# Optimization experiments

Hardware: AMD Instinct MI355X
Metric: run time of the kernel (lower is better)

The kernel has to match this reference:

```python
import jax, jax.numpy as jnp
import numpy as np

B, N, D = 4, 4096, 1024
HEADS, DIM_HEAD = 16, 64
INNER = HEADS * DIM_HEAD
LN_EPS = 1e-5


def next_fast_len(n):
    # smallest 5-smooth integer >= n (matches scipy.fftpack.next_fast_len)
    while True:
        m = n
        for p in (2, 3, 5):
            while m % p == 0:
                m //= p
        if m == 1:
            return n
        n += 1


def setup_inputs() -> dict:
    key = jax.random.key(0)
    k = jax.random.split(key, 6)
    x = jax.random.normal(k[0], (B, N, D), dtype=jnp.float32)
    gamma = jnp.ones((D,), dtype=jnp.float32)
    beta = jnp.zeros((D,), dtype=jnp.float32)
    alpha = jax.random.normal(k[1], (HEADS,), dtype=jnp.float32)
    w_in = jax.random.normal(k[2], (INNER, D), dtype=jnp.float32) * 0.02
    w_out = jax.random.normal(k[3], (D, INNER), dtype=jnp.float32) * 0.02
    return {"x": x, "gamma": gamma, "beta": beta, "alpha": alpha, "w_in": w_in, "w_out": w_out}


def reference(x, gamma, beta, alpha, w_in, w_out):
    b, n, d = x.shape
    h, dh = HEADS, DIM_HEAD
    # LayerNorm (biased variance, eps=1e-5)
    mu = jnp.mean(x, axis=-1, keepdims=True)
    var = jnp.var(x, axis=-1, keepdims=True)
    xn = (x - mu) * jax.lax.rsqrt(var + LN_EPS) * gamma + beta
    # project_in (no bias), split heads: b n (h d) -> b h n d
    xi = jnp.einsum('bnd,ed->bne', xn, w_in)
    xi = xi.reshape(b, n, h, dh).transpose(0, 2, 1, 3)  # [b,h,n,dh]
    # exponential decay weights per head: alpha * (1-alpha)**flip(arange(n)) -> [h, n]
    a = jax.nn.sigmoid(alpha)[:, None]
    weights = a * (1.0 - a) ** jnp.arange(n - 1, -1, -1, dtype=x.dtype)[None, :]
    # FFT-based causal correlation (conv1d_fft)
    fast_len = next_fast_len(n + n - 1)
    f_x = jnp.fft.rfft(xi, n=fast_len, axis=-2)           # [b,h,L',dh] complex
    f_w = jnp.fft.rfft(weights, n=fast_len, axis=-1)      # [h,L'] complex
    out = jnp.fft.irfft(f_x * jnp.conj(f_w)[None, :, :, None], fast_len, axis=-2)
    out = jnp.roll(out, -1, axis=-2)
    out = out[:, :, fast_len - n:, :]                      # last n positions -> [b,h,n,dh]
    # merge heads and project out
    out = out.transpose(0, 2, 1, 3).reshape(b, n, h * dh)
    return jnp.einsum('bne,de->bnd', out, w_out)
```

## Files before the change

### kernel.cpp

```cpp
#include <hip/hip_runtime.h>
#include <hip/hip_bf16.h>

#define B_ 4
#define N_ 4096
#define D_ 1024
#define H_ 16
#define INNER_ 1024
#define M_ (B_ * N_)
#define CH_ 128
#define CL_ 32

using bf16x8  = __attribute__((ext_vector_type(8))) __bf16;
using f32x4   = __attribute__((ext_vector_type(4))) float;
using f32x16  = __attribute__((ext_vector_type(16))) float;

__device__ __forceinline__ float bf2f(unsigned short v) {
  return __uint_as_float(((unsigned)v) << 16);
}
__device__ __forceinline__ unsigned short f2bf(float f) {
  __hip_bfloat16 h = __float2bfloat16(f);
  return *reinterpret_cast<unsigned short*>(&h);
}
__device__ __forceinline__ float sigm(float x) { return 1.f / (1.f + expf(-x)); }

__device__ __forceinline__ void gload_lds16(const void* g, void* l) {
  __builtin_amdgcn_global_load_lds(
      (const __attribute__((address_space(1))) unsigned int*)g,
      (__attribute__((address_space(3))) unsigned int*)l, 16, 0, 0);
}

#define W4_ ((INNER_ * D_) / 4)
__global__ __launch_bounds__(256) void lncast_kernel(
    const float* __restrict__ x, const float* __restrict__ gamma,
    const float* __restrict__ beta, __hip_bfloat16* __restrict__ xn,
    const float* __restrict__ wa, const float* __restrict__ wb,
    __hip_bfloat16* __restrict__ oa, __hip_bfloat16* __restrict__ ob) {
  if (blockIdx.x < 2048) {
    int i = blockIdx.x * 256 + threadIdx.x;
    const float* src = (i < W4_) ? wa : wb;
    __hip_bfloat16* dst = (i < W4_) ? oa : ob;
    int j = (i < W4_) ? i : i - W4_;
    float4 v = reinterpret_cast<const float4*>(src)[j];
    ushort4 o;
    o.x = f2bf(v.x); o.y = f2bf(v.y); o.z = f2bf(v.z); o.w = f2bf(v.w);
    reinterpret_cast<ushort4*>(dst)[j] = o;
    return;
  }
  const long row = blockIdx.x - 2048;
  const int t = threadIdx.x;
  const float4 v = reinterpret_cast<const float4*>(x + row * D_)[t];
  float s = v.x + v.y + v.z + v.w;
  float s2 = v.x * v.x + v.y * v.y + v.z * v.z + v.w * v.w;
#pragma unroll
  for (int o = 32; o > 0; o >>= 1) {
    s += __shfl_down(s, o);
    s2 += __shfl_down(s2, o);
  }
  __shared__ float red[8];
  const int lane = t & 63, wv = t >> 6;
  if (lane == 0) { red[wv] = s; red[4 + wv] = s2; }
  __syncthreads();
  const float sum = red[0] + red[1] + red[2] + red[3];
  const float sum2 = red[4] + red[5] + red[6] + red[7];
  const float mu = sum * (1.f / D_);
  const float var = sum2 * (1.f / D_) - mu * mu;
  const float rs = rsqrtf(var + 1e-5f);
  const float4 g = reinterpret_cast<const float4*>(gamma)[t];
  const float4 bb = reinterpret_cast<const float4*>(beta)[t];
  ushort4 o;
  o.x = f2bf((v.x - mu) * rs * g.x + bb.x);
  o.y = f2bf((v.y - mu) * rs * g.y + bb.y);
  o.z = f2bf((v.z - mu) * rs * g.z + bb.z);
  o.w = f2bf((v.w - mu) * rs * g.w + bb.w);
  reinterpret_cast<ushort4*>(xn + row * D_)[t] = o;
}

__device__ __forceinline__ void stc(float* p, float v) { *p = v; }
__device__ __forceinline__ void stc(__hip_bfloat16* p, float v) { *p = __float2bfloat16(v); }

template <typename TOUT, int NT>
__global__ __launch_bounds__(512) void gemm256_kernel(
    const __hip_bfloat16* __restrict__ A, const __hip_bfloat16* __restrict__ Bt,
    TOUT* __restrict__ C, int M, int N, int K) {
  static_assert(NT >= 4, "ring needs >=4 tiles");
  __shared__ __align__(16) char lds[131072];
  const int tid = threadIdx.x;
  const int lane = tid & 63;
  const int wave = tid >> 6;

  int wg = blockIdx.y * gridDim.x + blockIdx.x;
  wg = (wg & 7) * 32 + (wg >> 3);
  const int bx = wg & 3;
  const int by = wg >> 2;
  const long bm = (long)by * 256;
  const long bn = (long)bx * 256;

  const int u0  = (tid & 7) ^ ((tid >> 3) & 7);
  const int r0  = 2 * (tid >> 3) + (u0 >> 2);
  const int ck0 = u0 & 3;
  const __hip_bfloat16* sA0 = A + (bm + r0) * (long)K + ck0 * 8;
  const __hip_bfloat16* sA1 = sA0 + 128l * K;
  const __hip_bfloat16* sB0 = Bt + (bn + r0) * (long)K + ck0 * 8;
  const __hip_bfloat16* sB1 = sB0 + 128l * K;
  char* dbase = (char*)lds + wave * 1024;

  const int wm = wave >> 2;
  const int wn = wave & 3;
  const int l31 = lane & 31;
  const int lh  = lane >> 5;
  const int ub = ((lane & 1) << 2) | lh;
  const int ux = (l31 >> 1) & 7;
  const int uk0 = (ub ^ ux) * 16;
  const int uk1 = ((ub | 2) ^ ux) * 16;
  const int pA = wm * 8192 + (l31 >> 1) * 128;
  const int pB = 16384 + wn * 4096 + (l31 >> 1) * 128;

  f32x16 acc[4][2] = {};

#define STAGE_A(kt) do { const int _s = (kt) & 3;                         \
    gload_lds16(sA0 + (long)(kt) * 32, dbase + _s * 32768);               \
    gload_lds16(sA1 + (long)(kt) * 32, dbase + _s * 32768 + 8192); } while (0)
#define STAGE_B(kt) do { const int _s = (kt) & 3;                         \
    gload_lds16(sB0 + (long)(kt) * 32, dbase + _s * 32768 + 16384);       \
    gload_lds16(sB1 + (long)(kt) * 32, dbase + _s * 32768 + 24576); } while (0)

  STAGE_A(0); STAGE_B(0);
  STAGE_A(1); STAGE_B(1);
  asm volatile("s_waitcnt vmcnt(4)" ::: "memory");
  asm volatile("s_barrier" ::: "memory");

#pragma unroll
  for (int t = 0; t < NT; ++t) {
    const char* base = (const char*)lds + (t & 3) * 32768;
    bf16x8 av[4][2], bv[2][2];
#pragma unroll
    for (int cb = 0; cb < 2; ++cb) {
      bv[cb][0] = *(const bf16x8*)(base + pB + cb * 2048 + uk0);
      bv[cb][1] = *(const bf16x8*)(base + pB + cb * 2048 + uk1);
    }
#pragma unroll
    for (int rb = 0; rb < 4; ++rb) {
      av[rb][0] = *(const bf16x8*)(base + pA + rb * 2048 + uk0);
      av[rb][1] = *(const bf16x8*)(base + pA + rb * 2048 + uk1);
    }
    if (t + 2 < NT) { STAGE_A(t + 2); STAGE_B(t + 2); }
#pragma unroll
    for (int ks = 0; ks < 2; ++ks)
#pragma unroll
      for (int rb = 0; rb < 4; ++rb)
#pragma unroll
        for (int cb = 0; cb < 2; ++cb)
          acc[rb][cb] = __builtin_amdgcn_mfma_f32_32x32x16_bf16(
              av[rb][ks], bv[cb][ks], acc[rb][cb], 0, 0, 0);
    if (t + 2 < NT)      asm volatile("s_waitcnt vmcnt(4)" ::: "memory");
    else if (t + 1 < NT) asm volatile("s_waitcnt vmcnt(0)" ::: "memory");
    if (t + 1 < NT)      asm volatile("s_barrier" ::: "memory");
  }
#undef STAGE_A
#undef STAGE_B

#pragma unroll
  for (int rb = 0; rb < 4; ++rb)
#pragma unroll
    for (int cb = 0; cb < 2; ++cb)
#pragma unroll
      for (int r = 0; r < 16; ++r) {
        const long row = bm + wm * 128 + rb * 32 + (r & 3) + 8 * (r >> 2) + 4 * lh;
        const long col = bn + wn * 64 + cb * 32 + l31;
        stc(&C[row * (long)N + col], acc[rb][cb][r]);
      }
}

__global__ __launch_bounds__(256) void scan_finals_kernel(
    const __hip_bfloat16* __restrict__ xi, float* __restrict__ finals,
    const float* __restrict__ alpha) {
  const int e0 = threadIdx.x * 4;
  const int c = blockIdx.y;
  const int b = blockIdx.z;
  const float a = sigm(alpha[e0 >> 6]);
  const float om = 1.f - a;
  long base = ((long)b * N_ + (long)c * CL_) * INNER_ + e0;
  float y0 = 0.f, y1 = 0.f, y2 = 0.f, y3 = 0.f;
  for (int t = 0; t < CL_; ++t) {
    ushort4 u = *(const ushort4*)(xi + base);
    y0 = om * y0 + a * bf2f(u.x);
    y1 = om * y1 + a * bf2f(u.y);
    y2 = om * y2 + a * bf2f(u.z);
    y3 = om * y3 + a * bf2f(u.w);
    base += INNER_;
  }
  float4 f4 = make_float4(y0, y1, y2, y3);
  *reinterpret_cast<float4*>(&finals[((long)b * CH_ + c) * INNER_ + e0]) = f4;
}

__global__ __launch_bounds__(256) void scan_carry_kernel(
    const float* __restrict__ finals, float* __restrict__ carries,
    const float* __restrict__ alpha) {
  const int g = blockIdx.x * 256 + threadIdx.x;
  const int b = g >> 10;
  const int e = g & 1023;
  const float a = sigm(alpha[e >> 6]);
  const float dc = powf(1.f - a, (float)CL_);
  float carry = 0.f;
  for (int c = 0; c < CH_; ++c) {
    const long idx = ((long)b * CH_ + c) * INNER_ + e;
    carries[idx] = carry;
    carry = finals[idx] + dc * carry;
  }
}

__global__ __launch_bounds__(256) void scan_apply_kernel(
    const __hip_bfloat16* __restrict__ xi, __hip_bfloat16* __restrict__ y,
    const float* __restrict__ carries, const float* __restrict__ alpha) {
  const int e0 = threadIdx.x * 4;
  const int c = blockIdx.y;
  const int b = blockIdx.z;
  const float a = sigm(alpha[e0 >> 6]);
  const float om = 1.f - a;
  const float4 cr = *reinterpret_cast<const float4*>(
      &carries[((long)b * CH_ + c) * INNER_ + e0]);
  float y0 = cr.x, y1 = cr.y, y2 = cr.z, y3 = cr.w;
  long base = ((long)b * N_ + (long)c * CL_) * INNER_ + e0;
  for (int t = 0; t < CL_; ++t) {
    ushort4 u = *(const ushort4*)(xi + base);
    y0 = om * y0 + a * bf2f(u.x);
    y1 = om * y1 + a * bf2f(u.y);
    y2 = om * y2 + a * bf2f(u.z);
    y3 = om * y3 + a * bf2f(u.w);
    ushort4 o;
    o.x = f2bf(y0); o.y = f2bf(y1); o.z = f2bf(y2); o.w = f2bf(y3);
    *(ushort4*)(y + base) = o;
    base += INNER_;
  }
}

extern "C" void kernel_launch(void* const* d_in, const int* in_sizes, int n_in,
                              void* d_out, int out_size, void* d_ws, size_t ws_size,
                              hipStream_t stream) {
  const float* x     = (const float*)d_in[0];
  const float* gamma = (const float*)d_in[1];
  const float* beta  = (const float*)d_in[2];
  const float* alpha = (const float*)d_in[3];
  const float* w_in  = (const float*)d_in[4];
  const float* w_out = (const float*)d_in[5];
  float* out = (float*)d_out;
  char* ws = (char*)d_ws;

  __hip_bfloat16* xn = (__hip_bfloat16*)ws;
  __hip_bfloat16* wi = (__hip_bfloat16*)(ws + (32l << 20));
  __hip_bfloat16* wo = (__hip_bfloat16*)(ws + (34l << 20));
  float* finals      = (float*)(ws + (36l << 20));
  float* carries     = (float*)(ws + (38l << 20));
  __hip_bfloat16* xi = (__hip_bfloat16*)d_out;

  lncast_kernel<<<2048 + M_, 256, 0, stream>>>(x, gamma, beta, xn, w_in, w_out, wi, wo);

  gemm256_kernel<__hip_bfloat16, 32>
      <<<dim3(INNER_ / 256, M_ / 256), 512, 0, stream>>>(xn, wi, xi, M_, INNER_, D_);

  __hip_bfloat16* y = xn;
  scan_finals_kernel<<<dim3(1, CH_, B_), 256, 0, stream>>>(xi, finals, alpha);
  scan_carry_kernel<<<(B_ * INNER_) / 256, 256, 0, stream>>>(finals, carries, alpha);
  scan_apply_kernel<<<dim3(1, CH_, B_), 256, 0, stream>>>(xi, y, carries, alpha);

  gemm256_kernel<float, 32>
      <<<dim3(D_ / 256, M_ / 256), 512, 0, stream>>>(y, wo, out, M_, D_, INNER_);
}
```

Before: 130.4 us.

## Fuse scan chunk-finals into the GEMM epilogue and use 16 waves per tile

```diff
diff --git a/kernel.cpp b/kernel.cpp
--- a/kernel.cpp
+++ b/kernel.cpp
@@ -78,10 +78,11 @@
 __device__ __forceinline__ void stc(float* p, float v) { *p = v; }
 __device__ __forceinline__ void stc(__hip_bfloat16* p, float v) { *p = __float2bfloat16(v); }
 
-template <typename TOUT, int NT>
-__global__ __launch_bounds__(512) void gemm256_kernel(
+template <typename TOUT, int NT, bool FUSE>
+__global__ __launch_bounds__(1024, 4) void gemm256_kernel(
     const __hip_bfloat16* __restrict__ A, const __hip_bfloat16* __restrict__ Bt,
-    TOUT* __restrict__ C, int M, int N, int K) {
+    TOUT* __restrict__ C, float* __restrict__ finals, const float* __restrict__ alpha,
+    int M, int N, int K) {
   static_assert(NT >= 4, "ring needs >=4 tiles");
   __shared__ __align__(16) char lds[131072];
   const int tid = threadIdx.x;
@@ -98,10 +99,8 @@
   const int u0  = (tid & 7) ^ ((tid >> 3) & 7);
   const int r0  = 2 * (tid >> 3) + (u0 >> 2);
   const int ck0 = u0 & 3;
-  const __hip_bfloat16* sA0 = A + (bm + r0) * (long)K + ck0 * 8;
-  const __hip_bfloat16* sA1 = sA0 + 128l * K;
-  const __hip_bfloat16* sB0 = Bt + (bn + r0) * (long)K + ck0 * 8;
-  const __hip_bfloat16* sB1 = sB0 + 128l * K;
+  const __hip_bfloat16* sA = A + (bm + r0) * (long)K + ck0 * 8;
+  const __hip_bfloat16* sB = Bt + (bn + r0) * (long)K + ck0 * 8;
   char* dbase = (char*)lds + wave * 1024;
 
   const int wm = wave >> 2;
@@ -112,34 +111,30 @@
   const int ux = (l31 >> 1) & 7;
   const int uk0 = (ub ^ ux) * 16;
   const int uk1 = ((ub | 2) ^ ux) * 16;
-  const int pA = wm * 8192 + (l31 >> 1) * 128;
+  const int pA = wm * 4096 + (l31 >> 1) * 128;
   const int pB = 16384 + wn * 4096 + (l31 >> 1) * 128;
 
-  f32x16 acc[4][2] = {};
-
-#define STAGE_A(kt) do { const int _s = (kt) & 3;                         \
-    gload_lds16(sA0 + (long)(kt) * 32, dbase + _s * 32768);               \
-    gload_lds16(sA1 + (long)(kt) * 32, dbase + _s * 32768 + 8192); } while (0)
-#define STAGE_B(kt) do { const int _s = (kt) & 3;                         \
-    gload_lds16(sB0 + (long)(kt) * 32, dbase + _s * 32768 + 16384);       \
-    gload_lds16(sB1 + (long)(kt) * 32, dbase + _s * 32768 + 24576); } while (0)
+  f32x16 acc[2][2] = {};
+
+#define STAGE_A(kt) gload_lds16(sA + (long)(kt) * 32, dbase + ((kt) & 3) * 32768)
+#define STAGE_B(kt) gload_lds16(sB + (long)(kt) * 32, dbase + ((kt) & 3) * 32768 + 16384)
 
   STAGE_A(0); STAGE_B(0);
   STAGE_A(1); STAGE_B(1);
-  asm volatile("s_waitcnt vmcnt(4)" ::: "memory");
+  asm volatile("s_waitcnt vmcnt(2)" ::: "memory");
   asm volatile("s_barrier" ::: "memory");
 
-#pragma unroll
+#pragma unroll 4
   for (int t = 0; t < NT; ++t) {
     const char* base = (const char*)lds + (t & 3) * 32768;
-    bf16x8 av[4][2], bv[2][2];
+    bf16x8 av[2][2], bv[2][2];
 #pragma unroll
     for (int cb = 0; cb < 2; ++cb) {
       bv[cb][0] = *(const bf16x8*)(base + pB + cb * 2048 + uk0);
       bv[cb][1] = *(const bf16x8*)(base + pB + cb * 2048 + uk1);
     }
 #pragma unroll
-    for (int rb = 0; rb < 4; ++rb) {
+    for (int rb = 0; rb < 2; ++rb) {
       av[rb][0] = *(const bf16x8*)(base + pA + rb * 2048 + uk0);
       av[rb][1] = *(const bf16x8*)(base + pA + rb * 2048 + uk1);
     }
@@ -147,12 +142,12 @@
 #pragma unroll
     for (int ks = 0; ks < 2; ++ks)
 #pragma unroll
-      for (int rb = 0; rb < 4; ++rb)
+      for (int rb = 0; rb < 2; ++rb)
 #pragma unroll
         for (int cb = 0; cb < 2; ++cb)
           acc[rb][cb] = __builtin_amdgcn_mfma_f32_32x32x16_bf16(
               av[rb][ks], bv[cb][ks], acc[rb][cb], 0, 0, 0);
-    if (t + 2 < NT)      asm volatile("s_waitcnt vmcnt(4)" ::: "memory");
+    if (t + 2 < NT)      asm volatile("s_waitcnt vmcnt(2)" ::: "memory");
     else if (t + 1 < NT) asm volatile("s_waitcnt vmcnt(0)" ::: "memory");
     if (t + 1 < NT)      asm volatile("s_barrier" ::: "memory");
   }
@@ -160,37 +155,40 @@
 #undef STAGE_B
 
 #pragma unroll
-  for (int rb = 0; rb < 4; ++rb)
+  for (int rb = 0; rb < 2; ++rb)
 #pragma unroll
     for (int cb = 0; cb < 2; ++cb)
 #pragma unroll
       for (int r = 0; r < 16; ++r) {
-        const long row = bm + wm * 128 + rb * 32 + (r & 3) + 8 * (r >> 2) + 4 * lh;
+        const long row = bm + wm * 64 + rb * 32 + (r & 3) + 8 * (r >> 2) + 4 * lh;
         const long col = bn + wn * 64 + cb * 32 + l31;
         stc(&C[row * (long)N + col], acc[rb][cb][r]);
       }
-}
-
-__global__ __launch_bounds__(256) void scan_finals_kernel(
-    const __hip_bfloat16* __restrict__ xi, float* __restrict__ finals,
-    const float* __restrict__ alpha) {
-  const int e0 = threadIdx.x * 4;
-  const int c = blockIdx.y;
-  const int b = blockIdx.z;
-  const float a = sigm(alpha[e0 >> 6]);
-  const float om = 1.f - a;
-  long base = ((long)b * N_ + (long)c * CL_) * INNER_ + e0;
-  float y0 = 0.f, y1 = 0.f, y2 = 0.f, y3 = 0.f;
-  for (int t = 0; t < CL_; ++t) {
-    ushort4 u = *(const ushort4*)(xi + base);
-    y0 = om * y0 + a * bf2f(u.x);
-    y1 = om * y1 + a * bf2f(u.y);
-    y2 = om * y2 + a * bf2f(u.z);
-    y3 = om * y3 + a * bf2f(u.w);
-    base += INNER_;
-  }
-  float4 f4 = make_float4(y0, y1, y2, y3);
-  *reinterpret_cast<float4*>(&finals[((long)b * CH_ + c) * INNER_ + e0]) = f4;
+
+  if constexpr (FUSE) {
+#pragma unroll
+    for (int rb = 0; rb < 2; ++rb)
+#pragma unroll
+      for (int cb = 0; cb < 2; ++cb) {
+        const long row0 = bm + wm * 64 + rb * 32;
+        const int e = (int)bn + wn * 64 + cb * 32 + l31;
+        const float a = sigm(alpha[e >> 6]);
+        const float lw = log2f(1.f - a);
+        float partial = 0.f;
+#pragma unroll
+        for (int r = 0; r < 16; ++r) {
+          const int rowc = (r & 3) + 8 * (r >> 2) + 4 * lh;
+          partial += exp2f((float)(31 - rowc) * lw) * acc[rb][cb][r];
+        }
+        partial *= a;
+        partial += __shfl_xor(partial, 32);
+        if (lh == 0) {
+          const long b = row0 >> 12;
+          const long c = (row0 >> 5) & 127;
+          finals[(b * CH_ + c) * INNER_ + e] = partial;
+        }
+      }
+  }
 }
 
 __global__ __launch_bounds__(256) void scan_carry_kernel(
@@ -255,14 +253,15 @@
 
   lncast_kernel<<<2048 + M_, 256, 0, stream>>>(x, gamma, beta, xn, w_in, w_out, wi, wo);
 
-  gemm256_kernel<__hip_bfloat16, 32>
-      <<<dim3(INNER_ / 256, M_ / 256), 512, 0, stream>>>(xn, wi, xi, M_, INNER_, D_);
+  gemm256_kernel<__hip_bfloat16, 32, true>
+      <<<dim3(INNER_ / 256, M_ / 256), 1024, 0, stream>>>(xn, wi, xi, finals, alpha,
+                                                          M_, INNER_, D_);
 
   __hip_bfloat16* y = xn;
-  scan_finals_kernel<<<dim3(1, CH_, B_), 256, 0, stream>>>(xi, finals, alpha);
   scan_carry_kernel<<<(B_ * INNER_) / 256, 256, 0, stream>>>(finals, carries, alpha);
   scan_apply_kernel<<<dim3(1, CH_, B_), 256, 0, stream>>>(xi, y, carries, alpha);
 
-  gemm256_kernel<float, 32>
-      <<<dim3(D_ / 256, M_ / 256), 512, 0, stream>>>(y, wo, out, M_, D_, INNER_);
-}
+  gemm256_kernel<float, 32, false>
+      <<<dim3(D_ / 256, M_ / 256), 1024, 0, stream>>>(y, wo, out, nullptr, nullptr,
+                                                      M_, D_, INNER_);
+}
```

Result: no change. 130.3 us (-0.1%).
